# Optimization experiments

Measured on AMD Instinct MI355X. Metric: run time of the kernel, lower is better.

The kernel has to match this reference:

```python
import jax, jax.numpy as jnp
import numpy as np

B, N, K = 8, 16384, 32
EPS = 1e-5


def setup_inputs() -> dict:
    key = jax.random.key(0)
    ks = jax.random.split(key, 11)
    xyz = jax.random.normal(ks[0], (B, N, 3), jnp.float32)
    intensity = jax.random.normal(ks[1], (B, 3, N), jnp.float32)
    indices = jax.random.randint(ks[2], (B, N, K), 0, N)
    # linear_p: Conv2d(3,3,1)+BN+ReLU, then Conv2d(3,1,1)
    w1 = jax.random.normal(ks[3], (3, 3), jnp.float32) * 0.3
    b1 = jax.random.normal(ks[4], (3,), jnp.float32) * 0.1
    gamma = jax.random.uniform(ks[5], (3,), jnp.float32, 0.5, 1.5)
    beta = jax.random.normal(ks[6], (3,), jnp.float32) * 0.1
    mean = jax.random.normal(ks[7], (3,), jnp.float32) * 0.1
    var = jax.random.uniform(ks[8], (3,), jnp.float32, 0.5, 1.5)
    w2 = jax.random.normal(ks[9], (1, 3), jnp.float32) * 0.3
    b2 = jax.random.normal(ks[10], (1,), jnp.float32) * 0.1
    return dict(xyz=xyz, intensity=intensity, indices=indices, w1=w1, b1=b1,
                gamma=gamma, beta=beta, mean=mean, var=var, w2=w2, b2=b2)


def reference(xyz, intensity, indices, w1, b1, gamma, beta, mean, var, w2, b2):
    # neighbor gathers (irregular access)
    xyz_nb = jax.vmap(lambda p, i: p[i])(xyz, indices)          # [B,N,K,3]
    i_nb = jax.vmap(lambda ft, i: ft[:, i])(intensity, indices)  # [B,3,N,K]
    # relative position + gaussian kernel
    pos = xyz_nb - xyz[:, :, None, :]                            # [B,N,K,3]
    pos_g = jnp.exp(-2.0 * pos * pos)
    pos_g = jnp.transpose(pos_g, (0, 3, 1, 2))                   # [B,3,N,K]
    # 1x1 conv (3->3) + eval-mode BN + ReLU
    h = jnp.einsum('oc,bcnk->bonk', w1, pos_g) + b1[None, :, None, None]
    scale = gamma / jnp.sqrt(var + EPS)
    h = (h - mean[None, :, None, None]) * scale[None, :, None, None] + beta[None, :, None, None]
    h = jax.nn.relu(h)
    # 1x1 conv (3->1), softmax over neighbors
    w = jnp.einsum('oc,bcnk->bonk', w2, h) + b2[None, :, None, None]  # [B,1,N,K]
    w = jax.nn.softmax(w, axis=-1)
    # weighted reduce over neighbors
    return jnp.sum(i_nb * w, axis=-1)                            # [B,3,N]
```

## Files before the change

kernel.cpp:

```cpp
#include <hip/hip_runtime.h>
#include <hip/hip_fp16.h>
#include <math.h>

#define PB 8
#define PN 16384
#define PK 32
#define PEPS 1e-5f

__device__ __forceinline__ uint2 pack3(float a, float b, float c) {
    union { __half2 h2[2]; uint2 u; } r;
    r.h2[0] = __halves2half2(__float2half_rn(a), __float2half_rn(b));
    r.h2[1] = __halves2half2(__float2half_rn(c), __float2half_rn(0.f));
    return r.u;
}

__global__ __launch_bounds__(512, 1) void sa_fused(
    const float* __restrict__ xyz,
    const float* __restrict__ intensity,
    const int*   __restrict__ indices,
    const float* __restrict__ w1, const float* __restrict__ b1,
    const float* __restrict__ gamma_, const float* __restrict__ beta_,
    const float* __restrict__ mean_, const float* __restrict__ var_,
    const float* __restrict__ w2, const float* __restrict__ b2,
    float* __restrict__ out)
{
    __shared__ uint4 sbuf[PN / 2];
    const uint2* sx = (const uint2*)sbuf;

    const int tid = threadIdx.x;
    const int q   = blockIdx.x * 512 + tid;
    const int b   = q >> 14;
    const int n   = q & (PN - 1);

    const float sc0 = gamma_[0] * rsqrtf(var_[0] + PEPS);
    const float sc1 = gamma_[1] * rsqrtf(var_[1] + PEPS);
    const float sc2 = gamma_[2] * rsqrtf(var_[2] + PEPS);
    const float A00 = w1[0] * sc0, A01 = w1[1] * sc0, A02 = w1[2] * sc0;
    const float A10 = w1[3] * sc1, A11 = w1[4] * sc1, A12 = w1[5] * sc1;
    const float A20 = w1[6] * sc2, A21 = w1[7] * sc2, A22 = w1[8] * sc2;
    const float d0 = (b1[0] - mean_[0]) * sc0 + beta_[0];
    const float d1 = (b1[1] - mean_[1]) * sc1 + beta_[1];
    const float d2 = (b1[2] - mean_[2]) * sc2 + beta_[2];
    const float w0 = w2[0], w1v = w2[1], w2v = w2[2];
    const float bias2 = b2[0];

    const float cx = xyz[3 * (size_t)q + 0];
    const float cy = xyz[3 * (size_t)q + 1];
    const float cz = xyz[3 * (size_t)q + 2];

    int idxs[32];
    {
        const int4* ip = (const int4*)(indices + (size_t)q * PK);
#pragma unroll
        for (int j = 0; j < 8; ++j) {
            const int4 v = ip[j];
            idxs[4 * j + 0] = v.x; idxs[4 * j + 1] = v.y;
            idxs[4 * j + 2] = v.z; idxs[4 * j + 3] = v.w;
        }
    }

    {
        const float4* xv = (const float4*)(xyz + (size_t)b * PN * 3);
#pragma unroll
        for (int j = 0; j < 8; ++j) {
            const int m = tid + j * 512;
            const float4 f0 = xv[3 * m + 0];
            const float4 f1 = xv[3 * m + 1];
            const float4 f2 = xv[3 * m + 2];
            union { uint2 u2[4]; uint4 u4[2]; } pk;
            pk.u2[0] = pack3(f0.x, f0.y, f0.z);
            pk.u2[1] = pack3(f0.w, f1.x, f1.y);
            pk.u2[2] = pack3(f1.z, f1.w, f2.x);
            pk.u2[3] = pack3(f2.y, f2.z, f2.w);
            sbuf[2 * m + 0] = pk.u4[0];
            sbuf[2 * m + 1] = pk.u4[1];
        }
    }
    __syncthreads();

    const float4* iv = (const float4*)(intensity + (size_t)b * 3 * PN);
    float4 pf[16];
#pragma unroll
    for (int j = 0; j < 16; ++j) pf[j] = iv[tid + j * 512];

    float ev[32];
    float s = 0.f;
#pragma unroll
    for (int k = 0; k < PK; ++k) {
        const uint2 xz = sx[idxs[k]];
        const float2 nxy = __half22float2(*(const __half2*)&xz.x);
        const float  nz  = __half2float(*(const __half*)&xz.y);

        const float px = nxy.x - cx;
        const float py = nxy.y - cy;
        const float pz = nz - cz;

        const float g0 = __expf(-2.f * px * px);
        const float g1 = __expf(-2.f * py * py);
        const float g2 = __expf(-2.f * pz * pz);

        float h0 = fmaf(A00, g0, fmaf(A01, g1, fmaf(A02, g2, d0)));
        float h1 = fmaf(A10, g0, fmaf(A11, g1, fmaf(A12, g2, d1)));
        float h2 = fmaf(A20, g0, fmaf(A21, g1, fmaf(A22, g2, d2)));
        h0 = fmaxf(h0, 0.f); h1 = fmaxf(h1, 0.f); h2 = fmaxf(h2, 0.f);
        const float logit = fmaf(w0, h0, fmaf(w1v, h1, fmaf(w2v, h2, bias2)));

        const float e = __expf(logit);
        ev[k] = e;
        s += e;
    }

    float4 pr2[8];
#pragma unroll
    for (int j = 0; j < 8; ++j) pr2[j] = iv[8192 + tid + j * 512];

    __syncthreads();

#pragma unroll
    for (int j = 0; j < 8; ++j) {
        const int m = tid + j * 512;
        const float4 f0 = pf[j];
        const float4 f1 = pf[j + 8];
        const float4 f2 = pr2[j];
        union { uint2 u2[4]; uint4 u4[2]; } pk;
        pk.u2[0] = pack3(f0.x, f1.x, f2.x);
        pk.u2[1] = pack3(f0.y, f1.y, f2.y);
        pk.u2[2] = pack3(f0.z, f1.z, f2.z);
        pk.u2[3] = pack3(f0.w, f1.w, f2.w);
        sbuf[2 * m + 0] = pk.u4[0];
        sbuf[2 * m + 1] = pk.u4[1];
    }
    __syncthreads();

    float a0 = 0.f, a1 = 0.f, a2 = 0.f;
#pragma unroll
    for (int k = 0; k < PK; ++k) {
        const uint2 it = sx[idxs[k]];
        const float2 i01 = __half22float2(*(const __half2*)&it.x);
        const float  i2v = __half2float(*(const __half*)&it.y);
        const float e = ev[k];
        a0 = fmaf(e, i01.x, a0);
        a1 = fmaf(e, i01.y, a1);
        a2 = fmaf(e, i2v,  a2);
    }

    const float inv = 1.f / s;
    float* ob = out + (size_t)b * 3 * PN;
    ob[0 * PN + n] = a0 * inv;
    ob[1 * PN + n] = a1 * inv;
    ob[2 * PN + n] = a2 * inv;
}

extern "C" void kernel_launch(void* const* d_in, const int* in_sizes, int n_in,
                              void* d_out, int out_size, void* d_ws, size_t ws_size,
                              hipStream_t stream) {
    const float* xyz       = (const float*)d_in[0];
    const float* intensity = (const float*)d_in[1];
    const int*   indices   = (const int*)d_in[2];
    const float* w1        = (const float*)d_in[3];
    const float* b1        = (const float*)d_in[4];
    const float* gamma_    = (const float*)d_in[5];
    const float* beta_     = (const float*)d_in[6];
    const float* mean_     = (const float*)d_in[7];
    const float* var_      = (const float*)d_in[8];
    const float* w2        = (const float*)d_in[9];
    const float* b2        = (const float*)d_in[10];
    float* out = (float*)d_out;

    const int points = PB * PN;
    sa_fused<<<points / 512, 512, 0, stream>>>(xyz, intensity, indices,
                                               w1, b1, gamma_, beta_, mean_,
                                               var_, w2, b2, out);
}
```

Before: 100.3 us.

## Pre-pack xyz and intensity to fp16 in a separate kernel, gather intensity from global

Adds a pre-pass kernel that converts xyz and intensity into packed half-precision buffers in the workspace. The main kernel then copies the already-packed xyz straight into shared memory. It gathers intensity neighbours directly from global memory (L2) inside the single softmax loop, so the second shared-memory fill, its extra barriers and the stored exponent array are gone. The cost is an extra kernel launch, a workspace round trip, and random 8-byte global gathers in place of LDS reads.

```diff
diff --git a/kernel.cpp b/kernel.cpp
--- a/kernel.cpp
+++ b/kernel.cpp
@@ -14,9 +14,44 @@
     return r.u;
 }
 
+__global__ __launch_bounds__(256) void sa_pack(
+    const float* __restrict__ xyz,
+    const float* __restrict__ intensity,
+    uint4* __restrict__ pxyz,
+    uint4* __restrict__ pint)
+{
+    const int t = blockIdx.x * 256 + threadIdx.x;
+    const int b = t >> 12;
+    const int m = t & 4095;
+
+    const float4* xv = (const float4*)(xyz + (size_t)b * PN * 3);
+    const float4 f0 = xv[3 * m + 0];
+    const float4 f1 = xv[3 * m + 1];
+    const float4 f2 = xv[3 * m + 2];
+    union { uint2 u2[4]; uint4 u4[2]; } pk;
+    pk.u2[0] = pack3(f0.x, f0.y, f0.z);
+    pk.u2[1] = pack3(f0.w, f1.x, f1.y);
+    pk.u2[2] = pack3(f1.z, f1.w, f2.x);
+    pk.u2[3] = pack3(f2.y, f2.z, f2.w);
+    pxyz[2 * t + 0] = pk.u4[0];
+    pxyz[2 * t + 1] = pk.u4[1];
+
+    const float4* iv = (const float4*)(intensity + (size_t)b * 3 * PN);
+    const float4 i0 = iv[m];
+    const float4 i1 = iv[4096 + m];
+    const float4 i2 = iv[8192 + m];
+    pk.u2[0] = pack3(i0.x, i1.x, i2.x);
+    pk.u2[1] = pack3(i0.y, i1.y, i2.y);
+    pk.u2[2] = pack3(i0.z, i1.z, i2.z);
+    pk.u2[3] = pack3(i0.w, i1.w, i2.w);
+    pint[2 * t + 0] = pk.u4[0];
+    pint[2 * t + 1] = pk.u4[1];
+}
+
 __global__ __launch_bounds__(512, 1) void sa_fused(
     const float* __restrict__ xyz,
-    const float* __restrict__ intensity,
+    const uint4* __restrict__ pxyz,
+    const uint2* __restrict__ pint,
     const int*   __restrict__ indices,
     const float* __restrict__ w1, const float* __restrict__ b1,
     const float* __restrict__ gamma_, const float* __restrict__ beta_,
@@ -60,34 +95,23 @@
     }
 
     {
-        const float4* xv = (const float4*)(xyz + (size_t)b * PN * 3);
+        const uint4* xv = pxyz + (size_t)b * (PN / 2);
 #pragma unroll
-        for (int j = 0; j < 8; ++j) {
+        for (int j = 0; j < 16; ++j) {
             const int m = tid + j * 512;
-            const float4 f0 = xv[3 * m + 0];
-            const float4 f1 = xv[3 * m + 1];
-            const float4 f2 = xv[3 * m + 2];
-            union { uint2 u2[4]; uint4 u4[2]; } pk;
-            pk.u2[0] = pack3(f0.x, f0.y, f0.z);
-            pk.u2[1] = pack3(f0.w, f1.x, f1.y);
-            pk.u2[2] = pack3(f1.z, f1.w, f2.x);
-            pk.u2[3] = pack3(f2.y, f2.z, f2.w);
-            sbuf[2 * m + 0] = pk.u4[0];
-            sbuf[2 * m + 1] = pk.u4[1];
+            sbuf[m] = xv[m];
         }
     }
     __syncthreads();
 
-    const float4* iv = (const float4*)(intensity + (size_t)b * 3 * PN);
-    float4 pf[16];
-#pragma unroll
-    for (int j = 0; j < 16; ++j) pf[j] = iv[tid + j * 512];
-
-    float ev[32];
-    float s = 0.f;
+    const uint2* ib = pint + (size_t)b * PN;
+    float s = 0.f, a0 = 0.f, a1 = 0.f, a2 = 0.f;
 #pragma unroll
     for (int k = 0; k < PK; ++k) {
-        const uint2 xz = sx[idxs[k]];
+        const int idx = idxs[k];
+        const uint2 xz = sx[idx];
+        const uint2 it = ib[idx];
+
         const float2 nxy = __half22float2(*(const __half2*)&xz.x);
         const float  nz  = __half2float(*(const __half*)&xz.y);
 
@@ -106,39 +130,9 @@
         const float logit = fmaf(w0, h0, fmaf(w1v, h1, fmaf(w2v, h2, bias2)));
 
         const float e = __expf(logit);
-        ev[k] = e;
-        s += e;
-    }
-
-    float4 pr2[8];
-#pragma unroll
-    for (int j = 0; j < 8; ++j) pr2[j] = iv[8192 + tid + j * 512];
-
-    __syncthreads();
-
-#pragma unroll
-    for (int j = 0; j < 8; ++j) {
-        const int m = tid + j * 512;
-        const float4 f0 = pf[j];
-        const float4 f1 = pf[j + 8];
-        const float4 f2 = pr2[j];
-        union { uint2 u2[4]; uint4 u4[2]; } pk;
-        pk.u2[0] = pack3(f0.x, f1.x, f2.x);
-        pk.u2[1] = pack3(f0.y, f1.y, f2.y);
-        pk.u2[2] = pack3(f0.z, f1.z, f2.z);
-        pk.u2[3] = pack3(f0.w, f1.w, f2.w);
-        sbuf[2 * m + 0] = pk.u4[0];
-        sbuf[2 * m + 1] = pk.u4[1];
-    }
-    __syncthreads();
-
-    float a0 = 0.f, a1 = 0.f, a2 = 0.f;
-#pragma unroll
-    for (int k = 0; k < PK; ++k) {
-        const uint2 it = sx[idxs[k]];
         const float2 i01 = __half22float2(*(const __half2*)&it.x);
         const float  i2v = __half2float(*(const __half*)&it.y);
-        const float e = ev[k];
+        s += e;
         a0 = fmaf(e, i01.x, a0);
         a1 = fmaf(e, i01.y, a1);
         a2 = fmaf(e, i2v,  a2);
@@ -168,7 +162,12 @@
     float* out = (float*)d_out;
 
     const int points = PB * PN;
-    sa_fused<<<points / 512, 512, 0, stream>>>(xyz, intensity, indices,
-                                               w1, b1, gamma_, beta_, mean_,
-                                               var_, w2, b2, out);
+
+    uint4* pxyz = (uint4*)d_ws;
+    uint4* pint = pxyz + (size_t)points / 2;
+
+    sa_pack<<<points / 4 / 256, 256, 0, stream>>>(xyz, intensity, pxyz, pint);
+    sa_fused<<<points / 512, 512, 0, stream>>>(xyz, pxyz, (const uint2*)pint,
+                                               indices, w1, b1, gamma_, beta_,
+                                               mean_, var_, w2, b2, out);
 }
```

Result: slower. 116.6 us (+16.2%).

## Interleave batches across blocks, use native exp2, defer intensity loads

Applied to the files above, without the earlier changes.

Block-to-batch mapping changes so consecutive blocks cycle through the 8 batches instead of covering one batch contiguously, which changes how concurrently running blocks share the per-batch xyz/intensity data in L2. The exponentials become hardware exp2 with log2(e) folded into the constants. All intensity loads now happen after the softmax loop rather than half of them being prefetched before it, which lowers register pressure but gives up overlap of those loads with the compute.

```diff
diff --git a/kernel.cpp b/kernel.cpp
--- a/kernel.cpp
+++ b/kernel.cpp
@@ -6,6 +6,11 @@
 #define PN 16384
 #define PK 32
 #define PEPS 1e-5f
+#define LOG2E 1.4426950408889634f
+
+__device__ __forceinline__ float fexp2(float x) {
+    return __builtin_amdgcn_exp2f(x);
+}
 
 __device__ __forceinline__ uint2 pack3(float a, float b, float c) {
     union { __half2 h2[2]; uint2 u; } r;
@@ -27,10 +32,11 @@
     __shared__ uint4 sbuf[PN / 2];
     const uint2* sx = (const uint2*)sbuf;
 
-    const int tid = threadIdx.x;
-    const int q   = blockIdx.x * 512 + tid;
-    const int b   = q >> 14;
-    const int n   = q & (PN - 1);
+    const int tid  = threadIdx.x;
+    const int b    = blockIdx.x & 7;
+    const int slot = blockIdx.x >> 3;
+    const int n    = slot * 512 + tid;
+    const int q    = b * PN + n;
 
     const float sc0 = gamma_[0] * rsqrtf(var_[0] + PEPS);
     const float sc1 = gamma_[1] * rsqrtf(var_[1] + PEPS);
@@ -41,8 +47,9 @@
     const float d0 = (b1[0] - mean_[0]) * sc0 + beta_[0];
     const float d1 = (b1[1] - mean_[1]) * sc1 + beta_[1];
     const float d2 = (b1[2] - mean_[2]) * sc2 + beta_[2];
-    const float w0 = w2[0], w1v = w2[1], w2v = w2[2];
-    const float bias2 = b2[0];
+    const float w0 = w2[0] * LOG2E, w1v = w2[1] * LOG2E, w2v = w2[2] * LOG2E;
+    const float bias2 = b2[0] * LOG2E;
+    const float CG = -2.0f * LOG2E;
 
     const float cx = xyz[3 * (size_t)q + 0];
     const float cy = xyz[3 * (size_t)q + 1];
@@ -78,11 +85,6 @@
     }
     __syncthreads();
 
-    const float4* iv = (const float4*)(intensity + (size_t)b * 3 * PN);
-    float4 pf[16];
-#pragma unroll
-    for (int j = 0; j < 16; ++j) pf[j] = iv[tid + j * 512];
-
     float ev[32];
     float s = 0.f;
 #pragma unroll
@@ -95,33 +97,38 @@
         const float py = nxy.y - cy;
         const float pz = nz - cz;
 
-        const float g0 = __expf(-2.f * px * px);
-        const float g1 = __expf(-2.f * py * py);
-        const float g2 = __expf(-2.f * pz * pz);
+        const float g0 = fexp2(CG * px * px);
+        const float g1 = fexp2(CG * py * py);
+        const float g2 = fexp2(CG * pz * pz);
 
         float h0 = fmaf(A00, g0, fmaf(A01, g1, fmaf(A02, g2, d0)));
         float h1 = fmaf(A10, g0, fmaf(A11, g1, fmaf(A12, g2, d1)));
         float h2 = fmaf(A20, g0, fmaf(A21, g1, fmaf(A22, g2, d2)));
         h0 = fmaxf(h0, 0.f); h1 = fmaxf(h1, 0.f); h2 = fmaxf(h2, 0.f);
-        const float logit = fmaf(w0, h0, fmaf(w1v, h1, fmaf(w2v, h2, bias2)));
-
-        const float e = __expf(logit);
+        const float e =
+            fexp2(fmaf(w0, h0, fmaf(w1v, h1, fmaf(w2v, h2, bias2))));
         ev[k] = e;
         s += e;
     }
 
-    float4 pr2[8];
+    const float4* iv = (const float4*)(intensity + (size_t)b * 3 * PN);
+    float4 r0[8], r1[8], r2[8];
 #pragma unroll
-    for (int j = 0; j < 8; ++j) pr2[j] = iv[8192 + tid + j * 512];
+    for (int j = 0; j < 8; ++j) {
+        const int m = tid + j * 512;
+        r0[j] = iv[m];
+        r1[j] = iv[4096 + m];
+        r2[j] = iv[8192 + m];
+    }
 
     __syncthreads();
 
 #pragma unroll
     for (int j = 0; j < 8; ++j) {
         const int m = tid + j * 512;
-        const float4 f0 = pf[j];
-        const float4 f1 = pf[j + 8];
-        const float4 f2 = pr2[j];
+        const float4 f0 = r0[j];
+        const float4 f1 = r1[j];
+        const float4 f2 = r2[j];
         union { uint2 u2[4]; uint4 u4[2]; } pk;
         pk.u2[0] = pack3(f0.x, f1.x, f2.x);
         pk.u2[1] = pack3(f0.y, f1.y, f2.y);
```

Result: no change. 102.2 us (+1.9%).
